# Kernel optimization log

Measured on AMD Instinct MI355X. Metric: run time of the kernel, lower is better.

The kernel has to match this reference:

```python
import jax, jax.numpy as jnp
import numpy as np
from jax import lax

B, C1, C2, CM, H, W, K = 8, 256, 256, 128, 80, 80, 3
N = K * K
PAD = 1
EPS = 1e-5  # nn.BatchNorm2d default eps


def _bn(x, g, b, m, v):
    # eval-mode BatchNorm2d, NCHW
    inv = g / jnp.sqrt(v + EPS)
    return x * inv[None, :, None, None] + (b - m * inv)[None, :, None, None]


def _conv1x1(x, w):  # w: [O, I]
    return jnp.einsum('bihw,oi->bohw', x, w)


def _conv3x3(x, w, b):  # w: [O, I, 3, 3]
    y = lax.conv_general_dilated(x, w, window_strides=(1, 1),
                                 padding=((PAD, PAD), (PAD, PAD)),
                                 dimension_numbers=('NCHW', 'OIHW', 'NCHW'))
    return y + b[None, :, None, None]


def _deform_conv2d(x, offset, mask, w, bias):
    # DCNv2 (torchvision deform_conv2d semantics), stride=1, pad=1, k=3.
    # x: [B,C,H,W]; offset: [B,2N,H,W] pairs (dy,dx) per kernel tap (row-major);
    # mask: [B,N,H,W]; w: [O,C,3,3]
    Bx, C, Hx, Wx = x.shape
    ky, kx = jnp.meshgrid(jnp.arange(K), jnp.arange(K), indexing='ij')
    ky = ky.reshape(N).astype(x.dtype)
    kx = kx.reshape(N).astype(x.dtype)
    off = offset.reshape(Bx, N, 2, Hx, Wx)
    # sampling positions [B,N,H,W]
    py = (jnp.arange(Hx, dtype=x.dtype)[None, None, :, None] - PAD
          + ky[None, :, None, None] + off[:, :, 0])
    px = (jnp.arange(Wx, dtype=x.dtype)[None, None, None, :] - PAD
          + kx[None, :, None, None] + off[:, :, 1])

    y0 = jnp.floor(py)
    x0 = jnp.floor(px)
    wy1 = py - y0  # frac weights
    wx1 = px - x0
    x_flat = x.reshape(Bx, C, Hx * Wx)

    def corner(yi, xi, wgt):
        valid = (yi >= 0) & (yi < Hx) & (xi >= 0) & (xi < Wx)
        yc = jnp.clip(yi, 0, Hx - 1).astype(jnp.int32)
        xc = jnp.clip(xi, 0, Wx - 1).astype(jnp.int32)
        idx = (yc * Wx + xc).reshape(Bx, 1, N * Hx * Wx)
        g = jnp.take_along_axis(x_flat, idx, axis=2).reshape(Bx, C, N, Hx, Wx)
        return g * (wgt * valid.astype(x.dtype))[:, None]

    sampled = (corner(y0, x0, (1 - wy1) * (1 - wx1))
               + corner(y0, x0 + 1, (1 - wy1) * wx1)
               + corner(y0 + 1, x0, wy1 * (1 - wx1))
               + corner(y0 + 1, x0 + 1, wy1 * wx1))
    sampled = sampled * mask[:, None]  # modulated (v2)
    out = jnp.einsum('bcnhw,ocn->bohw', sampled, w.reshape(w.shape[0], C, N))
    return out + bias[None, :, None, None]


def setup_inputs() -> dict:
    key = jax.random.key(0)
    ks = jax.random.split(key, 20)
    f32 = jnp.float32
    d = {}
    d['x'] = jax.random.normal(ks[0], (B, C1, H, W), dtype=f32)
    # cv1: 1x1 conv (no bias) + BN
    d['cv1_w'] = jax.random.normal(ks[1], (CM, C1), dtype=f32) * (1.0 / np.sqrt(C1))
    d['bn1_g'] = jax.random.uniform(ks[2], (CM,), dtype=f32, minval=0.5, maxval=1.5)
    d['bn1_b'] = jax.random.normal(ks[3], (CM,), dtype=f32) * 0.1
    d['bn1_m'] = jax.random.normal(ks[4], (CM,), dtype=f32) * 0.1
    d['bn1_v'] = jax.random.uniform(ks[5], (CM,), dtype=f32, minval=0.5, maxval=1.5)
    # offset conv: predicts 3*N channels (2N offsets + N mask logits)
    d['off_w'] = jax.random.normal(ks[6], (3 * N, CM, K, K), dtype=f32) * 0.01
    d['off_b'] = jax.random.normal(ks[7], (3 * N,), dtype=f32) * 0.1
    # deformable conv main weight/bias
    d['dcn_w'] = jax.random.normal(ks[8], (CM, CM, K, K), dtype=f32) * np.sqrt(2.0 / (CM * N))
    d['dcn_b'] = jnp.zeros((CM,), dtype=f32)
    d['bn2_g'] = jax.random.uniform(ks[9], (CM,), dtype=f32, minval=0.5, maxval=1.5)
    d['bn2_b'] = jax.random.normal(ks[10], (CM,), dtype=f32) * 0.1
    d['bn2_m'] = jax.random.normal(ks[11], (CM,), dtype=f32) * 0.1
    d['bn2_v'] = jax.random.uniform(ks[12], (CM,), dtype=f32, minval=0.5, maxval=1.5)
    # cv3: 1x1 conv + BN
    d['cv3_w'] = jax.random.normal(ks[13], (C2, CM), dtype=f32) * (1.0 / np.sqrt(CM))
    d['bn3_g'] = jax.random.uniform(ks[14], (C2,), dtype=f32, minval=0.5, maxval=1.5)
    d['bn3_b'] = jax.random.normal(ks[15], (C2,), dtype=f32) * 0.1
    d['bn3_m'] = jax.random.normal(ks[16], (C2,), dtype=f32) * 0.1
    d['bn3_v'] = jax.random.uniform(ks[17], (C2,), dtype=f32, minval=0.5, maxval=1.5)
    return d


def reference(x, cv1_w, bn1_g, bn1_b, bn1_m, bn1_v,
              off_w, off_b, dcn_w, dcn_b,
              bn2_g, bn2_b, bn2_m, bn2_v,
              cv3_w, bn3_g, bn3_b, bn3_m, bn3_v):
    y = jax.nn.silu(_bn(_conv1x1(x, cv1_w), bn1_g, bn1_b, bn1_m, bn1_v))
    pred = _conv3x3(y, off_w, off_b)          # [B,3N,H,W]
    offset = pred[:, :2 * N]
    mask = jax.nn.sigmoid(pred[:, 2 * N:])
    y = _deform_conv2d(y, offset, mask, dcn_w, dcn_b)
    y = jax.nn.silu(_bn(y, bn2_g, bn2_b, bn2_m, bn2_v))
    y = jax.nn.silu(_bn(_conv1x1(y, cv3_w), bn3_g, bn3_b, bn3_m, bn3_v))
    return x + y  # shortcut: c1 == c2
```

## Files before the change

### kernel.cpp

```cpp
#include <hip/hip_runtime.h>
#include <math.h>

#define HWX   6400
#define WID   80
#define HGT   80
#define CMID  128
#define CIN   256
#define COUT  256

#define WS_BN   0
#define WS_Y2   1024
#define WS_Z2   3277824
#define WS_WPK  6554624
#define WS_WPO  6628352
#define WS_WP1  6646784
#define WS_WP3  6663168

typedef float floatx16 __attribute__((ext_vector_type(16)));
typedef short shortx8  __attribute__((ext_vector_type(8)));
typedef float floatx2  __attribute__((ext_vector_type(2)));

union U8 { uint32_t u[4]; shortx8 s; };

__device__ __forceinline__ float silu_f(float t){ return t / (1.f + __expf(-t)); }
__device__ __forceinline__ uint32_t f2bf(float f){
    uint32_t u = __float_as_uint(f);
    return (u + 0x7fffu + ((u >> 16) & 1u)) >> 16;
}
__device__ __forceinline__ floatx2 up2(uint32_t u){
    floatx2 r; r.x = __uint_as_float(u << 16); r.y = __uint_as_float(u & 0xffff0000u); return r;
}
__device__ __forceinline__ uint32_t pk2(floatx2 v){
    return __builtin_amdgcn_perm(__float_as_uint(v.y) + 0x8000u,
                                 __float_as_uint(v.x) + 0x8000u, 0x07060302u);
}
__device__ __forceinline__ uint32_t pk2f(float a, float b){ floatx2 v; v.x=a; v.y=b; return pk2(v); }

__device__ __forceinline__ uint4 blend4(uint4 u0, uint4 u1, uint4 u2, uint4 u3, float4 Wp){
    floatx2 W0, W1, W2, W3;
    W0.x = W0.y = Wp.x; W1.x = W1.y = Wp.y;
    W2.x = W2.y = Wp.z; W3.x = W3.y = Wp.w;
    uint4 r; floatx2 a;
    a = up2(u0.x)*W0;
    a = __builtin_elementwise_fma(up2(u1.x), W1, a);
    a = __builtin_elementwise_fma(up2(u2.x), W2, a);
    a = __builtin_elementwise_fma(up2(u3.x), W3, a); r.x = pk2(a);
    a = up2(u0.y)*W0;
    a = __builtin_elementwise_fma(up2(u1.y), W1, a);
    a = __builtin_elementwise_fma(up2(u2.y), W2, a);
    a = __builtin_elementwise_fma(up2(u3.y), W3, a); r.y = pk2(a);
    a = up2(u0.z)*W0;
    a = __builtin_elementwise_fma(up2(u1.z), W1, a);
    a = __builtin_elementwise_fma(up2(u2.z), W2, a);
    a = __builtin_elementwise_fma(up2(u3.z), W3, a); r.z = pk2(a);
    a = up2(u0.w)*W0;
    a = __builtin_elementwise_fma(up2(u1.w), W1, a);
    a = __builtin_elementwise_fma(up2(u2.w), W2, a);
    a = __builtin_elementwise_fma(up2(u3.w), W3, a); r.w = pk2(a);
    return r;
}

__global__ __launch_bounds__(256) void k0_prep(
    const float* __restrict__ dcn_w, const float* __restrict__ off_w,
    const float* __restrict__ cv1_w, const float* __restrict__ cv3_w,
    const float* __restrict__ g1, const float* __restrict__ b1, const float* __restrict__ m1, const float* __restrict__ v1,
    const float* __restrict__ g2, const float* __restrict__ b2, const float* __restrict__ m2, const float* __restrict__ v2,
    const float* __restrict__ dcn_b,
    const float* __restrict__ g3, const float* __restrict__ b3, const float* __restrict__ m3, const float* __restrict__ v3,
    uint32_t* __restrict__ wpk, uint32_t* __restrict__ wpo,
    uint32_t* __restrict__ wp1, uint32_t* __restrict__ wp3, float* __restrict__ bnw)
{
    int i = blockIdx.x * 256 + threadIdx.x;
    if (i < 4*9*8*256) {
        int j = i & 3, lane = (i >> 2) & 63, s = (i >> 8) & 7;
        int r2 = i >> 11; int tap = r2 % 9, g = r2 / 9;
        int oc = g*32 + (lane & 31);
        int c  = s*16 + ((lane >> 5) << 3) + 2*j;
        wpk[i] = f2bf(dcn_w[(oc*128 + c)*9 + tap]) | (f2bf(dcn_w[(oc*128 + c + 1)*9 + tap]) << 16);
    }
    if (i < 9*8*256) {
        int j = i & 3, lane = (i >> 2) & 63, s = (i >> 8) & 7, tap = i >> 11;
        int oc = lane & 31;
        int c  = s*16 + ((lane >> 5) << 3) + 2*j;
        float lo = (oc < 27) ? off_w[(oc*128 + c)*9 + tap] : 0.f;
        float hi = (oc < 27) ? off_w[(oc*128 + c + 1)*9 + tap] : 0.f;
        wpo[i] = f2bf(lo) | (f2bf(hi) << 16);
    }
    if (i < 4*16*256) {
        int j = i & 3, lane = (i >> 2) & 63, s = (i >> 8) & 15, g = i >> 12;
        int oc = g*32 + (lane & 31);
        int c  = s*16 + ((lane >> 5) << 3) + 2*j;
        wp1[i] = f2bf(cv1_w[oc*256 + c]) | (f2bf(cv1_w[oc*256 + c + 1]) << 16);
    }
    if (i < 8*8*256) {
        int j = i & 3, lane = (i >> 2) & 63, s = (i >> 8) & 7, g = i >> 11;
        int oc = g*32 + (lane & 31);
        int c  = s*16 + ((lane >> 5) << 3) + 2*j;
        wp3[i] = f2bf(cv3_w[oc*128 + c]) | (f2bf(cv3_w[oc*128 + c + 1]) << 16);
    }
    if (i < 128) {
        float inv = g1[i] * rsqrtf(v1[i] + 1e-5f);
        bnw[i] = inv; bnw[128+i] = b1[i] - m1[i]*inv;
    } else if (i < 256) {
        int j = i - 128;
        float inv = g2[j] * rsqrtf(v2[j] + 1e-5f);
        bnw[256+j] = inv; bnw[384+j] = b2[j] - m2[j]*inv + inv*dcn_b[j];
    } else if (i < 512) {
        int j = i - 256;
        float inv = g3[j] * rsqrtf(v3[j] + 1e-5f);
        bnw[512+j] = inv; bnw[768+j] = b3[j] - m3[j]*inv;
    }
}

#define K1PAD 68
__global__ __launch_bounds__(256) void k1_cv1(
    const float* __restrict__ x, const uint32_t* __restrict__ wp1,
    const float* __restrict__ bn, uint32_t* __restrict__ y2)
{
    __shared__ __align__(16) uint32_t L[64*66];
    int i0 = blockIdx.x;
    int blk = (i0 & 7) * 100 + (i0 >> 3);
    int b = blk / 100, pix0 = (blk % 100) * 64;
    int t = threadIdx.x;
    int lane = t & 63, w = t >> 6;
    int pixl = lane & 31, bhalf = lane >> 5;
    floatx16 acc0 = {}, acc1 = {};
    const float* xb = x + (size_t)b*CIN*HWX + pix0;
    const uint32_t* wpg = wp1 + (size_t)(w*16)*256 + lane*4;

    int r2 = t >> 4, c4 = (t & 15) * 4;
    for (int kk = 0; kk < 256; kk += 32) {
        float4 a0 = *(const float4*)(xb + (size_t)(kk + 2*r2)*HWX + c4);
        float4 a1 = *(const float4*)(xb + (size_t)(kk + 2*r2 + 1)*HWX + c4);
        uint4 q;
        q.x = pk2f(a0.x, a1.x);
        q.y = pk2f(a0.y, a1.y);
        q.z = pk2f(a0.z, a1.z);
        q.w = pk2f(a0.w, a1.w);
        __syncthreads();
        *(uint4*)&L[r2*K1PAD + c4] = q;
        __syncthreads();
        #pragma unroll
        for (int sl = 0; sl < 2; sl++) {
            int s = (kk >> 4) + sl;
            U8 a, b0, b1;
            const uint32_t* as = wpg + s*256;
            a.u[0]=as[0]; a.u[1]=as[1]; a.u[2]=as[2]; a.u[3]=as[3];
            int row = sl*8 + bhalf*4;
            #pragma unroll
            for (int j = 0; j < 4; j++) b0.u[j] = L[(row+j)*K1PAD + pixl];
            #pragma unroll
            for (int j = 0; j < 4; j++) b1.u[j] = L[(row+j)*K1PAD + 32 + pixl];
            acc0 = __builtin_amdgcn_mfma_f32_32x32x16_bf16(a.s, b0.s, acc0, 0, 0, 0);
            acc1 = __builtin_amdgcn_mfma_f32_32x32x16_bf16(a.s, b1.s, acc1, 0, 0, 0);
        }
    }
    __syncthreads();
    #pragma unroll
    for (int r = 0; r < 16; r += 2) {
        int oc = w*32 + (r & 3) + 8*(r >> 2) + 4*bhalf;
        float s0 = bn[oc],   be0 = bn[128+oc];
        float s1 = bn[oc+1], be1 = bn[128+oc+1];
        uint32_t d0 = pk2f(silu_f(acc0[r]*s0+be0), silu_f(acc0[r+1]*s1+be1));
        uint32_t d1 = pk2f(silu_f(acc1[r]*s0+be0), silu_f(acc1[r+1]*s1+be1));
        int oc2 = oc >> 1;
        L[pixl*66 + oc2]        = d0;
        L[(32+pixl)*66 + oc2]   = d1;
    }
    __syncthreads();
    uint32_t* y2b = y2 + (size_t)b*HWX*64 + (size_t)pix0*64;
    int q2 = t & 31, p0 = t >> 5;
    #pragma unroll
    for (int pp = 0; pp < 8; pp++) {
        int pix = p0 + pp*8;
        uint2 v = make_uint2(L[pix*66 + q2*2], L[pix*66 + q2*2 + 1]);
        *(uint2*)(y2b + (size_t)pix*64 + q2*2) = v;
    }
}

#define S2R 68
__global__ __launch_bounds__(256) void k3_dcn(
    const uint32_t* __restrict__ y2, const uint32_t* __restrict__ wpo,
    const float* __restrict__ ob,
    const uint32_t* __restrict__ wpk, const float* __restrict__ bn, uint32_t* __restrict__ z2)
{
    __shared__ __align__(16) uint32_t S2[2][32*S2R];
    __shared__ __align__(16) int   sidx9[9*32*4];
    __shared__ __align__(16) float swgt9[9*32*4];
    int i0 = blockIdx.x;
    int blk = (i0 & 7) * 200 + (i0 >> 3);
    int b = blk / 200, pix0 = (blk % 200) * 32;
    int t = threadIdx.x;
    int lane = t & 63, w = t >> 6;
    int pixl = lane & 31, bhalf = lane >> 5;
    const uint32_t* yb = y2 + (size_t)b*HWX*64;
    floatx16 acc = {};
    float* LF = (float*)&S2[0][0];

    {
        floatx16 accp = {};
        int tap0 = (w < 3) ? w*2 : 6;
        int ntap = (w < 3) ? 2 : 3;
        int p = pix0 + pixl;
        int h = p / WID, xw = p % WID;
        for (int tt = 0; tt < ntap; tt++) {
            int tap = tap0 + tt;
            int gh = h + tap/3 - 1, gx = xw + tap%3 - 1;
            bool valid = (gh >= 0) && (gh < HGT) && (gx >= 0) && (gx < WID);
            const uint32_t* pp2 = yb + (size_t)(gh*WID + gx)*64 + bhalf*4;
            const uint32_t* ap = wpo + (size_t)(tap*8)*256 + lane*4;
            #pragma unroll
            for (int s = 0; s < 8; s++) {
                U8 a, bf;
                const uint32_t* as = ap + s*256;
                a.u[0]=as[0]; a.u[1]=as[1]; a.u[2]=as[2]; a.u[3]=as[3];
                if (valid) {
                    uint4 q = *(const uint4*)(pp2 + s*8);
                    bf.u[0]=q.x; bf.u[1]=q.y; bf.u[2]=q.z; bf.u[3]=q.w;
                } else {
                    bf.u[0]=0u; bf.u[1]=0u; bf.u[2]=0u; bf.u[3]=0u;
                }
                accp = __builtin_amdgcn_mfma_f32_32x32x16_bf16(a.s, bf.s, accp, 0, 0, 0);
            }
        }
        #pragma unroll
        for (int r = 0; r < 16; r++) {
            int oc = (r & 3) + 8*(r >> 2) + 4*bhalf;
            LF[w*1024 + oc*32 + pixl] = accp[r];
        }
    }
    __syncthreads();
    #pragma unroll
    for (int k = 0; k < 4; k++) {
        int e = t + 256*k;
        int oc = e >> 5;
        float v = LF[e] + LF[1024+e] + LF[2048+e] + LF[3072+e];
        if (oc < 27) {
            v += ob[oc];
            if (oc >= 18) v = 1.f/(1.f+__expf(-v));
        }
        LF[e] = v;
    }
    __syncthreads();

    for (int it = t; it < 288; it += 256) {
        int tap = it >> 5, px = it & 31;
        int pix = pix0 + px;
        int h = pix / WID, wq = pix % WID;
        float dy = LF[(2*tap)*32 + px];
        float dx = LF[(2*tap+1)*32 + px];
        float mk = LF[(18+tap)*32 + px];
        float pyf = (float)(h - 1 + tap/3) + dy;
        float pxf = (float)(wq - 1 + tap%3) + dx;
        float y0f = floorf(pyf), x0f = floorf(pxf);
        float wy1 = pyf - y0f, wx1 = pxf - x0f;
        int iy0 = (int)y0f, ix0 = (int)x0f;
        int iy1 = iy0 + 1,  ix1 = ix0 + 1;
        float vy0 = (iy0 >= 0 && iy0 < HGT) ? 1.f : 0.f;
        float vy1 = (iy1 >= 0 && iy1 < HGT) ? 1.f : 0.f;
        float vx0 = (ix0 >= 0 && ix0 < WID) ? 1.f : 0.f;
        float vx1 = (ix1 >= 0 && ix1 < WID) ? 1.f : 0.f;
        int cy0 = min(max(iy0,0),HGT-1), cy1 = min(max(iy1,0),HGT-1);
        int cx0 = min(max(ix0,0),WID-1), cx1 = min(max(ix1,0),WID-1);
        int base = (tap*32 + px)*4;
        sidx9[base+0] = cy0*WID+cx0; sidx9[base+1] = cy0*WID+cx1;
        sidx9[base+2] = cy1*WID+cx0; sidx9[base+3] = cy1*WID+cx1;
        swgt9[base+0] = (1.f-wy1)*(1.f-wx1)*mk*vy0*vx0;
        swgt9[base+1] = (1.f-wy1)*wx1*mk*vy0*vx1;
        swgt9[base+2] = wy1*(1.f-wx1)*mk*vy1*vx0;
        swgt9[base+3] = wy1*wx1*mk*vy1*vx1;
    }
    __syncthreads();

    uint4  u[2][4];
    float4 W[2];
    uint4  samp[2];
    int c8 = lane & 15, pg = lane >> 4;

    #pragma unroll
    for (int p = 0; p < 2; p++) {
        int pix = w*8 + p*4 + pg;
        int base = (0*32 + pix)*4;
        int4 si = *(const int4*)&sidx9[base];
        W[p] = *(const float4*)&swgt9[base];
        u[p][0] = *(const uint4*)(yb + (size_t)si.x*64 + c8*4);
        u[p][1] = *(const uint4*)(yb + (size_t)si.y*64 + c8*4);
        u[p][2] = *(const uint4*)(yb + (size_t)si.z*64 + c8*4);
        u[p][3] = *(const uint4*)(yb + (size_t)si.w*64 + c8*4);
    }
    #pragma unroll
    for (int p = 0; p < 2; p++)
        samp[p] = blend4(u[p][0], u[p][1], u[p][2], u[p][3], W[p]);

    #pragma unroll
    for (int tap = 0; tap < 9; tap++) {
        uint32_t* S = &S2[tap & 1][0];
        #pragma unroll
        for (int p = 0; p < 2; p++) {
            int pix = w*8 + p*4 + pg;
            *(uint4*)&S[pix*S2R + c8*4] = samp[p];
        }
        __syncthreads();
        if (tap < 8) {
            #pragma unroll
            for (int p = 0; p < 2; p++) {
                int pix = w*8 + p*4 + pg;
                int base = ((tap+1)*32 + pix)*4;
                int4 si = *(const int4*)&sidx9[base];
                W[p] = *(const float4*)&swgt9[base];
                u[p][0] = *(const uint4*)(yb + (size_t)si.x*64 + c8*4);
                u[p][1] = *(const uint4*)(yb + (size_t)si.y*64 + c8*4);
                u[p][2] = *(const uint4*)(yb + (size_t)si.z*64 + c8*4);
                u[p][3] = *(const uint4*)(yb + (size_t)si.w*64 + c8*4);
            }
        }
        const uint32_t* wp = wpk + (size_t)((w*9 + tap)*8)*256 + lane*4;
        #pragma unroll
        for (int s = 0; s < 8; s++) {
            U8 a, bf;
            const uint32_t* wps = wp + s*256;
            a.u[0] = wps[0]; a.u[1] = wps[1]; a.u[2] = wps[2]; a.u[3] = wps[3];
            uint4 q = *(const uint4*)&S[pixl*S2R + s*8 + bhalf*4];
            bf.u[0]=q.x; bf.u[1]=q.y; bf.u[2]=q.z; bf.u[3]=q.w;
            acc = __builtin_amdgcn_mfma_f32_32x32x16_bf16(a.s, bf.s, acc, 0, 0, 0);
        }
        if (tap < 8) {
            #pragma unroll
            for (int p = 0; p < 2; p++)
                samp[p] = blend4(u[p][0], u[p][1], u[p][2], u[p][3], W[p]);
        }
    }
    uint32_t* SE = &S2[1][0];
    #pragma unroll
    for (int r = 0; r < 16; r += 2) {
        int oc = w*32 + (r & 3) + 8*(r >> 2) + 4*bhalf;
        float s0 = bn[256+oc],   be0 = bn[384+oc];
        float s1 = bn[256+oc+1], be1 = bn[384+oc+1];
        SE[pixl*S2R + (oc >> 1)] = pk2f(silu_f(acc[r]*s0+be0), silu_f(acc[r+1]*s1+be1));
    }
    __syncthreads();
    uint32_t* z2b = z2 + (size_t)b*HWX*64 + (size_t)pix0*64;
    int q2 = t & 31, p0 = t >> 5;
    #pragma unroll
    for (int pp = 0; pp < 4; pp++) {
        int pix = p0 + pp*8;
        uint2 v = *(const uint2*)&SE[pix*S2R + q2*2];
        *(uint2*)(z2b + (size_t)pix*64 + q2*2) = v;
    }
}

__global__ __launch_bounds__(256) void k4_cv3(
    const uint32_t* __restrict__ z2, const uint32_t* __restrict__ wp3,
    const float* __restrict__ bn, const float* __restrict__ x, float* __restrict__ out)
{
    int i0 = blockIdx.x;
    int blk = (i0 & 7) * 200 + (i0 >> 3);
    int half = blk & 1, blk2 = blk >> 1;
    int b = blk2 / 100, pix0 = (blk2 % 100) * 64;
    int t = threadIdx.x;
    int lane = t & 63, w = t >> 6;
    int pixl = lane & 31, bhalf = lane >> 5;
    int g = half*4 + w;
    floatx16 acc0 = {}, acc1 = {};
    const uint32_t* zb = z2 + (size_t)b*HWX*64 + (size_t)pix0*64;
    const uint32_t* wpg = wp3 + (size_t)(g*8)*256 + lane*4;

    #pragma unroll
    for (int s = 0; s < 8; s++) {
        U8 a, b0, b1;
        const uint32_t* as = wpg + s*256;
        a.u[0]=as[0]; a.u[1]=as[1]; a.u[2]=as[2]; a.u[3]=as[3];
        uint4 q0 = *(const uint4*)(zb + (size_t)pixl*64 + s*8 + bhalf*4);
        uint4 q1 = *(const uint4*)(zb + (size_t)(32+pixl)*64 + s*8 + bhalf*4);
        b0.u[0]=q0.x; b0.u[1]=q0.y; b0.u[2]=q0.z; b0.u[3]=q0.w;
        b1.u[0]=q1.x; b1.u[1]=q1.y; b1.u[2]=q1.z; b1.u[3]=q1.w;
        acc0 = __builtin_amdgcn_mfma_f32_32x32x16_bf16(a.s, b0.s, acc0, 0, 0, 0);
        acc1 = __builtin_amdgcn_mfma_f32_32x32x16_bf16(a.s, b1.s, acc1, 0, 0, 0);
    }
    const float* xb = x + (size_t)b*COUT*HWX + pix0;
    float* ob = out + (size_t)b*COUT*HWX + pix0;
    #pragma unroll
    for (int r = 0; r < 16; r++) {
        int oc = g*32 + (r & 3) + 8*(r >> 2) + 4*bhalf;
        float sc = bn[512+oc], be = bn[768+oc];
        float v0 = silu_f(acc0[r]*sc+be) + xb[(size_t)oc*HWX + pixl];
        float v1 = silu_f(acc1[r]*sc+be) + xb[(size_t)oc*HWX + 32 + pixl];
        ob[(size_t)oc*HWX + pixl]      = v0;
        ob[(size_t)oc*HWX + 32 + pixl] = v1;
    }
}

extern "C" void kernel_launch(void* const* d_in, const int* in_sizes, int n_in,
                              void* d_out, int out_size, void* d_ws, size_t ws_size,
                              hipStream_t stream) {
    const float* x     = (const float*)d_in[0];
    const float* cv1_w = (const float*)d_in[1];
    const float* bn1_g = (const float*)d_in[2];
    const float* bn1_b = (const float*)d_in[3];
    const float* bn1_m = (const float*)d_in[4];
    const float* bn1_v = (const float*)d_in[5];
    const float* off_w = (const float*)d_in[6];
    const float* off_b = (const float*)d_in[7];
    const float* dcn_w = (const float*)d_in[8];
    const float* dcn_b = (const float*)d_in[9];
    const float* bn2_g = (const float*)d_in[10];
    const float* bn2_b = (const float*)d_in[11];
    const float* bn2_m = (const float*)d_in[12];
    const float* bn2_v = (const float*)d_in[13];
    const float* cv3_w = (const float*)d_in[14];
    const float* bn3_g = (const float*)d_in[15];
    const float* bn3_b = (const float*)d_in[16];
    const float* bn3_m = (const float*)d_in[17];
    const float* bn3_v = (const float*)d_in[18];

    float* ws   = (float*)d_ws;
    float*    BN   = ws + WS_BN;
    uint32_t* Y2   = (uint32_t*)(ws + WS_Y2);
    uint32_t* Z2   = (uint32_t*)(ws + WS_Z2);
    uint32_t* WPK  = (uint32_t*)(ws + WS_WPK);
    uint32_t* WPO  = (uint32_t*)(ws + WS_WPO);
    uint32_t* WP1  = (uint32_t*)(ws + WS_WP1);
    uint32_t* WP3  = (uint32_t*)(ws + WS_WP3);

    hipLaunchKernelGGL(k0_prep, dim3(288), dim3(256), 0, stream,
        dcn_w, off_w, cv1_w, cv3_w,
        bn1_g, bn1_b, bn1_m, bn1_v,
        bn2_g, bn2_b, bn2_m, bn2_v, dcn_b,
        bn3_g, bn3_b, bn3_m, bn3_v, WPK, WPO, WP1, WP3, BN);
    hipLaunchKernelGGL(k1_cv1, dim3(800), dim3(256), 0, stream, x, WP1, BN, Y2);
    hipLaunchKernelGGL(k3_dcn, dim3(1600), dim3(256), 0, stream, Y2, WPO, off_b, WPK, BN, Z2);
    hipLaunchKernelGGL(k4_cv3, dim3(1600), dim3(256), 0, stream, Z2, WP3, BN, x, (float*)d_out);
}
```

Measured before the change: 221.6 us.

## Process two DCN taps per barrier stage in deformable conv kernel

Restructures the tap loop of the DCN kernel so that each pipeline stage gathers and blends two kernel taps at once, using four shared-memory sample buffers instead of two. This halves the number of __syncthreads barriers and issues twice as many gather loads in flight per stage, to better hide gather latency behind the MFMA work. In exchange it doubles the register footprint for prefetched corners and the LDS use for sample buffers, which may reduce occupancy.

Result: no change. 220.8 us (-0.3%).

```diff
diff --git a/kernel.cpp b/kernel.cpp
--- a/kernel.cpp
+++ b/kernel.cpp
@@ -184,7 +184,7 @@
     const float* __restrict__ ob,
     const uint32_t* __restrict__ wpk, const float* __restrict__ bn, uint32_t* __restrict__ z2)
 {
-    __shared__ __align__(16) uint32_t S2[2][32*S2R];
+    __shared__ __align__(16) uint32_t S2[4][32*S2R];
     __shared__ __align__(16) int   sidx9[9*32*4];
     __shared__ __align__(16) float swgt9[9*32*4];
     int i0 = blockIdx.x;
@@ -272,62 +272,79 @@
     }
     __syncthreads();
 
-    uint4  u[2][4];
-    float4 W[2];
-    uint4  samp[2];
+    uint4  u[4][4];
+    float4 W[4];
+    uint4  samp[4];
     int c8 = lane & 15, pg = lane >> 4;
 
     #pragma unroll
-    for (int p = 0; p < 2; p++) {
+    for (int i = 0; i < 4; i++) {
+        int tp = i >> 1, p = i & 1;
         int pix = w*8 + p*4 + pg;
-        int base = (0*32 + pix)*4;
+        int base = (tp*32 + pix)*4;
         int4 si = *(const int4*)&sidx9[base];
-        W[p] = *(const float4*)&swgt9[base];
-        u[p][0] = *(const uint4*)(yb + (size_t)si.x*64 + c8*4);
-        u[p][1] = *(const uint4*)(yb + (size_t)si.y*64 + c8*4);
-        u[p][2] = *(const uint4*)(yb + (size_t)si.z*64 + c8*4);
-        u[p][3] = *(const uint4*)(yb + (size_t)si.w*64 + c8*4);
-    }
-    #pragma unroll
-    for (int p = 0; p < 2; p++)
-        samp[p] = blend4(u[p][0], u[p][1], u[p][2], u[p][3], W[p]);
-
-    #pragma unroll
-    for (int tap = 0; tap < 9; tap++) {
-        uint32_t* S = &S2[tap & 1][0];
+        W[i] = *(const float4*)&swgt9[base];
+        u[i][0] = *(const uint4*)(yb + (size_t)si.x*64 + c8*4);
+        u[i][1] = *(const uint4*)(yb + (size_t)si.y*64 + c8*4);
+        u[i][2] = *(const uint4*)(yb + (size_t)si.z*64 + c8*4);
+        u[i][3] = *(const uint4*)(yb + (size_t)si.w*64 + c8*4);
+    }
+    #pragma unroll
+    for (int i = 0; i < 4; i++)
+        samp[i] = blend4(u[i][0], u[i][1], u[i][2], u[i][3], W[i]);
+
+    #pragma unroll
+    for (int r = 0; r < 5; r++) {
         #pragma unroll
-        for (int p = 0; p < 2; p++) {
-            int pix = w*8 + p*4 + pg;
-            *(uint4*)&S[pix*S2R + c8*4] = samp[p];
+        for (int i = 0; i < 4; i++) {
+            int tp = i >> 1, p = i & 1;
+            if (2*r + tp < 9) {
+                int pix = w*8 + p*4 + pg;
+                *(uint4*)&S2[(r & 1)*2 + tp][pix*S2R + c8*4] = samp[i];
+            }
         }
         __syncthreads();
-        if (tap < 8) {
+        if (r < 4) {
             #pragma unroll
-            for (int p = 0; p < 2; p++) {
-                int pix = w*8 + p*4 + pg;
-                int base = ((tap+1)*32 + pix)*4;
-                int4 si = *(const int4*)&sidx9[base];
-                W[p] = *(const float4*)&swgt9[base];
-                u[p][0] = *(const uint4*)(yb + (size_t)si.x*64 + c8*4);
-                u[p][1] = *(const uint4*)(yb + (size_t)si.y*64 + c8*4);
-                u[p][2] = *(const uint4*)(yb + (size_t)si.z*64 + c8*4);
-                u[p][3] = *(const uint4*)(yb + (size_t)si.w*64 + c8*4);
+            for (int i = 0; i < 4; i++) {
+                int tp = i >> 1, p = i & 1;
+                int tap = 2*r + 2 + tp;
+                if (tap < 9) {
+                    int pix = w*8 + p*4 + pg;
+                    int base = (tap*32 + pix)*4;
+                    int4 si = *(const int4*)&sidx9[base];
+                    W[i] = *(const float4*)&swgt9[base];
+                    u[i][0] = *(const uint4*)(yb + (size_t)si.x*64 + c8*4);
+                    u[i][1] = *(const uint4*)(yb + (size_t)si.y*64 + c8*4);
+                    u[i][2] = *(const uint4*)(yb + (size_t)si.z*64 + c8*4);
+                    u[i][3] = *(const uint4*)(yb + (size_t)si.w*64 + c8*4);
+                }
             }
         }
-        const uint32_t* wp = wpk + (size_t)((w*9 + tap)*8)*256 + lane*4;
         #pragma unroll
-        for (int s = 0; s < 8; s++) {
-            U8 a, bf;
-            const uint32_t* wps = wp + s*256;
-            a.u[0] = wps[0]; a.u[1] = wps[1]; a.u[2] = wps[2]; a.u[3] = wps[3];
-            uint4 q = *(const uint4*)&S[pixl*S2R + s*8 + bhalf*4];
-            bf.u[0]=q.x; bf.u[1]=q.y; bf.u[2]=q.z; bf.u[3]=q.w;
-            acc = __builtin_amdgcn_mfma_f32_32x32x16_bf16(a.s, bf.s, acc, 0, 0, 0);
-        }
-        if (tap < 8) {
+        for (int tp = 0; tp < 2; tp++) {
+            int tap = 2*r + tp;
+            if (tap < 9) {
+                const uint32_t* wp = wpk + (size_t)((w*9 + tap)*8)*256 + lane*4;
+                const uint32_t* Sb = &S2[(r & 1)*2 + tp][0];
+                #pragma unroll
+                for (int s = 0; s < 8; s++) {
+                    U8 a, bf;
+                    const uint32_t* wps = wp + s*256;
+                    a.u[0] = wps[0]; a.u[1] = wps[1]; a.u[2] = wps[2]; a.u[3] = wps[3];
+                    uint4 q = *(const uint4*)&Sb[pixl*S2R + s*8 + bhalf*4];
+                    bf.u[0]=q.x; bf.u[1]=q.y; bf.u[2]=q.z; bf.u[3]=q.w;
+                    acc = __builtin_amdgcn_mfma_f32_32x32x16_bf16(a.s, bf.s, acc, 0, 0, 0);
+                }
+            }
+        }
+        if (r < 4) {
             #pragma unroll
-            for (int p = 0; p < 2; p++)
-                samp[p] = blend4(u[p][0], u[p][1], u[p][2], u[p][3], W[p]);
+            for (int i = 0; i < 4; i++) {
+                int tp = i >> 1;
+                if (2*r + 2 + tp < 9)
+                    samp[i] = blend4(u[i][0], u[i][1], u[i][2], u[i][3], W[i]);
+            }
         }
     }
     uint32_t* SE = &S2[1][0];
```

## Fuse cv3 1x1 conv and residual epilogue into the DCN kernel

Applied to the files above, without the earlier changes.

The final 1x1 conv (cv3), its BN+SiLU and the residual add now run inside the deformable-conv kernel. They read the bf16 activations straight from shared memory instead of writing the z2 intermediate to global memory and launching a separate kernel. This removes one launch and a global round trip of the intermediate tensor. In exchange each 32-pixel block now does all 256 output channels, which adds per-wave MFMA work and register pressure, and the output and residual stores become 32-wide, less coalesced runs.

Result: faster. 207.8 us (-6.2%).

```diff
diff --git a/kernel.cpp b/kernel.cpp
--- a/kernel.cpp
+++ b/kernel.cpp
@@ -182,7 +182,9 @@
 __global__ __launch_bounds__(256) void k3_dcn(
     const uint32_t* __restrict__ y2, const uint32_t* __restrict__ wpo,
     const float* __restrict__ ob,
-    const uint32_t* __restrict__ wpk, const float* __restrict__ bn, uint32_t* __restrict__ z2)
+    const uint32_t* __restrict__ wpk, const float* __restrict__ bn,
+    const uint32_t* __restrict__ wp3, const float* __restrict__ x,
+    float* __restrict__ outp)
 {
     __shared__ __align__(16) uint32_t S2[2][32*S2R];
     __shared__ __align__(16) int   sidx9[9*32*4];
@@ -339,54 +341,33 @@
         SE[pixl*S2R + (oc >> 1)] = pk2f(silu_f(acc[r]*s0+be0), silu_f(acc[r+1]*s1+be1));
     }
     __syncthreads();
-    uint32_t* z2b = z2 + (size_t)b*HWX*64 + (size_t)pix0*64;
-    int q2 = t & 31, p0 = t >> 5;
-    #pragma unroll
-    for (int pp = 0; pp < 4; pp++) {
-        int pix = p0 + pp*8;
-        uint2 v = *(const uint2*)&SE[pix*S2R + q2*2];
-        *(uint2*)(z2b + (size_t)pix*64 + q2*2) = v;
-    }
-}
-
-__global__ __launch_bounds__(256) void k4_cv3(
-    const uint32_t* __restrict__ z2, const uint32_t* __restrict__ wp3,
-    const float* __restrict__ bn, const float* __restrict__ x, float* __restrict__ out)
-{
-    int i0 = blockIdx.x;
-    int blk = (i0 & 7) * 200 + (i0 >> 3);
-    int half = blk & 1, blk2 = blk >> 1;
-    int b = blk2 / 100, pix0 = (blk2 % 100) * 64;
-    int t = threadIdx.x;
-    int lane = t & 63, w = t >> 6;
-    int pixl = lane & 31, bhalf = lane >> 5;
-    int g = half*4 + w;
-    floatx16 acc0 = {}, acc1 = {};
-    const uint32_t* zb = z2 + (size_t)b*HWX*64 + (size_t)pix0*64;
-    const uint32_t* wpg = wp3 + (size_t)(g*8)*256 + lane*4;
-
+
+    floatx16 c0 = {}, c1 = {};
     #pragma unroll
     for (int s = 0; s < 8; s++) {
-        U8 a, b0, b1;
-        const uint32_t* as = wpg + s*256;
-        a.u[0]=as[0]; a.u[1]=as[1]; a.u[2]=as[2]; a.u[3]=as[3];
-        uint4 q0 = *(const uint4*)(zb + (size_t)pixl*64 + s*8 + bhalf*4);
-        uint4 q1 = *(const uint4*)(zb + (size_t)(32+pixl)*64 + s*8 + bhalf*4);
-        b0.u[0]=q0.x; b0.u[1]=q0.y; b0.u[2]=q0.z; b0.u[3]=q0.w;
-        b1.u[0]=q1.x; b1.u[1]=q1.y; b1.u[2]=q1.z; b1.u[3]=q1.w;
-        acc0 = __builtin_amdgcn_mfma_f32_32x32x16_bf16(a.s, b0.s, acc0, 0, 0, 0);
-        acc1 = __builtin_amdgcn_mfma_f32_32x32x16_bf16(a.s, b1.s, acc1, 0, 0, 0);
+        U8 a0, a1, bf;
+        const uint32_t* w0 = wp3 + (size_t)(w*8 + s)*256 + lane*4;
+        const uint32_t* w1 = wp3 + (size_t)((w+4)*8 + s)*256 + lane*4;
+        a0.u[0]=w0[0]; a0.u[1]=w0[1]; a0.u[2]=w0[2]; a0.u[3]=w0[3];
+        a1.u[0]=w1[0]; a1.u[1]=w1[1]; a1.u[2]=w1[2]; a1.u[3]=w1[3];
+        uint4 q = *(const uint4*)&SE[pixl*S2R + s*8 + bhalf*4];
+        bf.u[0]=q.x; bf.u[1]=q.y; bf.u[2]=q.z; bf.u[3]=q.w;
+        c0 = __builtin_amdgcn_mfma_f32_32x32x16_bf16(a0.s, bf.s, c0, 0, 0, 0);
+        c1 = __builtin_amdgcn_mfma_f32_32x32x16_bf16(a1.s, bf.s, c1, 0, 0, 0);
     }
     const float* xb = x + (size_t)b*COUT*HWX + pix0;
-    float* ob = out + (size_t)b*COUT*HWX + pix0;
+    float* obp = outp + (size_t)b*COUT*HWX + pix0;
     #pragma unroll
     for (int r = 0; r < 16; r++) {
-        int oc = g*32 + (r & 3) + 8*(r >> 2) + 4*bhalf;
-        float sc = bn[512+oc], be = bn[768+oc];
-        float v0 = silu_f(acc0[r]*sc+be) + xb[(size_t)oc*HWX + pixl];
-        float v1 = silu_f(acc1[r]*sc+be) + xb[(size_t)oc*HWX + 32 + pixl];
-        ob[(size_t)oc*HWX + pixl]      = v0;
-        ob[(size_t)oc*HWX + 32 + pixl] = v1;
+        int ocl = (r & 3) + 8*(r >> 2) + 4*bhalf;
+        int oc0 = w*32 + ocl;
+        int oc1 = 128 + w*32 + ocl;
+        float sc0 = bn[512+oc0], be0 = bn[768+oc0];
+        float sc1 = bn[512+oc1], be1 = bn[768+oc1];
+        float v0 = silu_f(c0[r]*sc0+be0) + xb[(size_t)oc0*HWX + pixl];
+        float v1 = silu_f(c1[r]*sc1+be1) + xb[(size_t)oc1*HWX + pixl];
+        obp[(size_t)oc0*HWX + pixl] = v0;
+        obp[(size_t)oc1*HWX + pixl] = v1;
     }
 }
 
@@ -416,7 +397,6 @@
     float* ws   = (float*)d_ws;
     float*    BN   = ws + WS_BN;
     uint32_t* Y2   = (uint32_t*)(ws + WS_Y2);
-    uint32_t* Z2   = (uint32_t*)(ws + WS_Z2);
     uint32_t* WPK  = (uint32_t*)(ws + WS_WPK);
     uint32_t* WPO  = (uint32_t*)(ws + WS_WPO);
     uint32_t* WP1  = (uint32_t*)(ws + WS_WP1);
@@ -428,6 +408,6 @@
         bn2_g, bn2_b, bn2_m, bn2_v, dcn_b,
         bn3_g, bn3_b, bn3_m, bn3_v, WPK, WPO, WP1, WP3, BN);
     hipLaunchKernelGGL(k1_cv1, dim3(800), dim3(256), 0, stream, x, WP1, BN, Y2);
-    hipLaunchKernelGGL(k3_dcn, dim3(1600), dim3(256), 0, stream, Y2, WPO, off_b, WPK, BN, Z2);
-    hipLaunchKernelGGL(k4_cv3, dim3(1600), dim3(256), 0, stream, Z2, WP3, BN, x, (float*)d_out);
-}
+    hipLaunchKernelGGL(k3_dcn, dim3(1600), dim3(256), 0, stream,
+        Y2, WPO, off_b, WPK, BN, WP3, x, (float*)d_out);
+}
```
